# Kernel optimization log

Hardware: AMD Instinct MI355X
Metric: run time of the kernel (lower is better)

## Reference

```python
import jax, jax.numpy as jnp
import numpy as np

N_NODES = 100000
N_EDGES = 3200000
D_IN = 256
D_OUT = 256


def setup_inputs() -> dict:
    key = jax.random.key(0)
    k1, k2, k3, k4, k5 = jax.random.split(key, 5)
    inputs = jax.random.normal(k1, (N_NODES, D_IN), dtype=jnp.float32)
    # Glorot-uniform init as in _glorot_init
    init_range = np.sqrt(6.0 / (D_IN + D_OUT)).astype(np.float32)
    weight = jax.random.uniform(k2, (D_IN, D_OUT), dtype=jnp.float32,
                                minval=-init_range, maxval=init_range)
    edge_src = jax.random.randint(k3, (N_EDGES,), 0, N_NODES, dtype=jnp.int32)
    edge_dst = jax.random.randint(k4, (N_EDGES,), 0, N_NODES, dtype=jnp.int32)
    # normalized adjacency values (positive, like D^-1/2 A D^-1/2 entries)
    edge_vals = jax.random.uniform(k5, (N_EDGES,), dtype=jnp.float32)
    return {"inputs": inputs, "weight": weight, "edge_src": edge_src,
            "edge_dst": edge_dst, "edge_vals": edge_vals}


def reference(inputs, weight, edge_src, edge_dst, edge_vals):
    # x = inputs @ W          : [N, D_OUT]
    x = inputs @ weight
    # SpMM: out[d] = sum_{e: dst(e)=d} vals[e] * x[src(e)]
    msgs = edge_vals[:, None] * x[edge_src]          # [E, D_OUT]
    out = jax.ops.segment_sum(msgs, edge_dst, num_segments=inputs.shape[0])
    return jax.nn.relu(out)
```

## Files before the change

### kernel.cpp

```cpp
#include <hip/hip_runtime.h>

#define N_NODES 100000
#define N_EDGES 3200000
#define DDIM 256
#define NB 1563
#define BIN_BLK 256
#define CHUNK (N_EDGES / BIN_BLK)

typedef short s16x8 __attribute__((ext_vector_type(8)));
typedef float f32x4 __attribute__((ext_vector_type(4)));

__device__ __forceinline__ unsigned short f32_to_bf16(float f) {
    union { float f; unsigned int u; } c; c.f = f;
    unsigned int u = c.u;
    unsigned int r = u + 0x7fffu + ((u >> 16) & 1u);
    return (unsigned short)(r >> 16);
}
__device__ __forceinline__ float bf16_to_f32(unsigned short h) {
    union { unsigned int u; float f; } c; c.u = ((unsigned int)h) << 16;
    return c.f;
}

__global__ __launch_bounds__(256) void prep_w(const float* __restrict__ W,
                                              unsigned short* __restrict__ Wt) {
    __shared__ float tile[32][33];
    const int tx = threadIdx.x & 31;
    const int ty = threadIdx.x >> 5;
    const int n0 = blockIdx.x * 32;
    const int k0 = blockIdx.y * 32;
    for (int i = 0; i < 32; i += 8)
        tile[ty + i][tx] = W[(size_t)(k0 + ty + i) * DDIM + n0 + tx];
    __syncthreads();
    for (int i = 0; i < 32; i += 8)
        Wt[(size_t)(n0 + ty + i) * DDIM + k0 + tx] = f32_to_bf16(tile[tx][ty + i]);
}

__global__ __launch_bounds__(256) void gemm_mfma(const float* __restrict__ A,
                                                 const unsigned short* __restrict__ Wt,
                                                 unsigned short* __restrict__ Xb) {
    __shared__ unsigned short As[64][DDIM + 8];
    const int tid = threadIdx.x;
    const int rowBase = blockIdx.x * 64;

#pragma unroll
    for (int p = 0; p < 16; ++p) {
        const int flat = p * 256 + tid;
        const int row = flat >> 6;
        const int k4 = (flat & 63) * 4;
        const int gr = rowBase + row;
        float4 v = make_float4(0.f, 0.f, 0.f, 0.f);
        if (gr < N_NODES) v = *(const float4*)&A[(size_t)gr * DDIM + k4];
        ushort4 h;
        h.x = f32_to_bf16(v.x); h.y = f32_to_bf16(v.y);
        h.z = f32_to_bf16(v.z); h.w = f32_to_bf16(v.w);
        *(ushort4*)&As[row][k4] = h;
    }
    __syncthreads();

    const int wave = tid >> 6;
    const int lane = tid & 63;
    const int lrow = lane & 15;
    const int quad = lane >> 4;
    const int cb = wave * 64;

    f32x4 acc[4][4] = {};

#pragma unroll
    for (int ks = 0; ks < 8; ++ks) {
        const int k0 = ks * 32 + quad * 8;
        s16x8 a[4], b[4];
#pragma unroll
        for (int ri = 0; ri < 4; ++ri)
            a[ri] = *(const s16x8*)&As[ri * 16 + lrow][k0];
#pragma unroll
        for (int ci = 0; ci < 4; ++ci)
            b[ci] = *(const s16x8*)&Wt[(size_t)(cb + ci * 16 + lrow) * DDIM + k0];
#pragma unroll
        for (int ri = 0; ri < 4; ++ri)
#pragma unroll
            for (int ci = 0; ci < 4; ++ci)
                acc[ri][ci] = __builtin_amdgcn_mfma_f32_16x16x32_bf16(a[ri], b[ci], acc[ri][ci], 0, 0, 0);
    }

#pragma unroll
    for (int ri = 0; ri < 4; ++ri) {
        const int r0 = rowBase + ri * 16 + quad * 4;
#pragma unroll
        for (int rr = 0; rr < 4; ++rr) {
            const int row = r0 + rr;
            if (row < N_NODES) {
#pragma unroll
                for (int ci = 0; ci < 4; ++ci)
                    Xb[(size_t)row * DDIM + cb + ci * 16 + lrow] = f32_to_bf16(acc[ri][ci][rr]);
            }
        }
    }
}

__global__ __launch_bounds__(256) void zero_small(int* __restrict__ p, int n) {
    int i = blockIdx.x * 256 + threadIdx.x;
    if (i < n) p[i] = 0;
}

__global__ __launch_bounds__(256) void hist_coarse(const int* __restrict__ edst,
                                                   int* __restrict__ gcounts) {
    __shared__ int h[NB];
    const int tid = threadIdx.x;
    for (int i = tid; i < NB; i += 256) h[i] = 0;
    __syncthreads();
    const int lo = blockIdx.x * CHUNK;
    const int hi = lo + CHUNK;
    for (int e = lo + tid; e < hi; e += 256) atomicAdd(&h[edst[e] >> 6], 1);
    __syncthreads();
    for (int i = tid; i < NB; i += 256)
        if (h[i]) atomicAdd(&gcounts[i], h[i]);
}

__global__ __launch_bounds__(256) void scan_coarse(const int* __restrict__ gcounts,
                                                   int* __restrict__ bbase,
                                                   int* __restrict__ bcursor,
                                                   int* __restrict__ off) {
    __shared__ int part[256];
    const int t = threadIdx.x;
    const int chunk = (NB + 255) / 256;
    const int lo = t * chunk;
    const int hi = min(lo + chunk, NB);
    int s = 0;
    for (int i = lo; i < hi; ++i) s += gcounts[i];
    part[t] = s;
    __syncthreads();
    for (int d = 1; d < 256; d <<= 1) {
        int a = (t >= d) ? part[t - d] : 0;
        __syncthreads();
        part[t] += a;
        __syncthreads();
    }
    int run = part[t] - s;
    for (int i = lo; i < hi; ++i) {
        bbase[i] = run;
        bcursor[i] = run;
        run += gcounts[i];
    }
    if (t == 255) {
        bbase[NB] = run;
        off[N_NODES] = run;
    }
}

__global__ __launch_bounds__(256) void bin_coarse(const int* __restrict__ esrc,
                                                  const int* __restrict__ edst,
                                                  const float* __restrict__ evals,
                                                  int* __restrict__ bcursor,
                                                  int2* __restrict__ tmp) {
    __shared__ int h[NB];
    __shared__ int sb[NB];
    const int tid = threadIdx.x;
    for (int i = tid; i < NB; i += 256) h[i] = 0;
    __syncthreads();
    const int lo = blockIdx.x * CHUNK;
    const int hi = lo + CHUNK;
    for (int e = lo + tid; e < hi; e += 256) atomicAdd(&h[edst[e] >> 6], 1);
    __syncthreads();
    for (int i = tid; i < NB; i += 256)
        sb[i] = h[i] ? atomicAdd(&bcursor[i], h[i]) : 0;
    __syncthreads();
    for (int e = lo + tid; e < hi; e += 256) {
        const int d = edst[e];
        const int b = d >> 6;
        const int p = atomicAdd(&sb[b], 1);
        tmp[p] = make_int2(esrc[e] | ((d & 63) << 17), __float_as_int(evals[e]));
    }
}

__global__ __launch_bounds__(256) void refine(const int2* __restrict__ tmp,
                                              const int* __restrict__ bbase,
                                              int* __restrict__ off,
                                              int2* __restrict__ srcval) {
    __shared__ int nh[64];
    __shared__ int nb[64];
    const int b = blockIdx.x;
    const int tid = threadIdx.x;
    const int base = bbase[b];
    const int cnt = bbase[b + 1] - base;
    const int n0 = b * 64;
    const int nn = min(64, N_NODES - n0);
    if (tid < 64) nh[tid] = 0;
    __syncthreads();
    for (int i = tid; i < cnt; i += 256)
        atomicAdd(&nh[tmp[base + i].x >> 17], 1);
    __syncthreads();
    if (tid == 0) {
        int run = 0;
        for (int i = 0; i < 64; ++i) { nb[i] = run; run += nh[i]; }
    }
    __syncthreads();
    if (tid < nn) off[n0 + tid] = base + nb[tid];
    __syncthreads();
    for (int i = tid; i < cnt; i += 256) {
        const int2 r = tmp[base + i];
        const int dl = r.x >> 17;
        const int p = atomicAdd(&nb[dl], 1);
        srcval[base + p] = make_int2(r.x & 0x1FFFF, r.y);
    }
}

__global__ __launch_bounds__(256) void spmm_gather(const unsigned short* __restrict__ xb,
                                                   const int* __restrict__ off,
                                                   const int2* __restrict__ srcval,
                                                   float* __restrict__ out) {
    const int node = blockIdx.x * 4 + (threadIdx.x >> 6);
    const int lane = threadIdx.x & 63;
    const int start = off[node];
    const int end = off[node + 1];

    float4 acc = make_float4(0.f, 0.f, 0.f, 0.f);

    for (int base = start; base < end; base += 64) {
        const int cnt = min(64, end - base);
        int s_l = 0;
        float v_l = 0.f;
        if (lane < cnt) {
            int2 p = srcval[base + lane];
            s_l = p.x;
            v_l = __int_as_float(p.y);
        }
        int j = 0;
        for (; j + 4 <= cnt; j += 4) {
            const int s0 = __shfl(s_l, j + 0);
            const int s1 = __shfl(s_l, j + 1);
            const int s2 = __shfl(s_l, j + 2);
            const int s3 = __shfl(s_l, j + 3);
            const float v0 = __shfl(v_l, j + 0);
            const float v1 = __shfl(v_l, j + 1);
            const float v2 = __shfl(v_l, j + 2);
            const float v3 = __shfl(v_l, j + 3);
            const ushort4 h0 = *(const ushort4*)&xb[(size_t)s0 * DDIM + lane * 4];
            const ushort4 h1 = *(const ushort4*)&xb[(size_t)s1 * DDIM + lane * 4];
            const ushort4 h2 = *(const ushort4*)&xb[(size_t)s2 * DDIM + lane * 4];
            const ushort4 h3 = *(const ushort4*)&xb[(size_t)s3 * DDIM + lane * 4];
            acc.x += v0 * bf16_to_f32(h0.x); acc.y += v0 * bf16_to_f32(h0.y);
            acc.z += v0 * bf16_to_f32(h0.z); acc.w += v0 * bf16_to_f32(h0.w);
            acc.x += v1 * bf16_to_f32(h1.x); acc.y += v1 * bf16_to_f32(h1.y);
            acc.z += v1 * bf16_to_f32(h1.z); acc.w += v1 * bf16_to_f32(h1.w);
            acc.x += v2 * bf16_to_f32(h2.x); acc.y += v2 * bf16_to_f32(h2.y);
            acc.z += v2 * bf16_to_f32(h2.z); acc.w += v2 * bf16_to_f32(h2.w);
            acc.x += v3 * bf16_to_f32(h3.x); acc.y += v3 * bf16_to_f32(h3.y);
            acc.z += v3 * bf16_to_f32(h3.z); acc.w += v3 * bf16_to_f32(h3.w);
        }
        for (; j < cnt; ++j) {
            const int s = __shfl(s_l, j);
            const float v = __shfl(v_l, j);
            const ushort4 h = *(const ushort4*)&xb[(size_t)s * DDIM + lane * 4];
            acc.x += v * bf16_to_f32(h.x); acc.y += v * bf16_to_f32(h.y);
            acc.z += v * bf16_to_f32(h.z); acc.w += v * bf16_to_f32(h.w);
        }
    }

    acc.x = fmaxf(acc.x, 0.f);
    acc.y = fmaxf(acc.y, 0.f);
    acc.z = fmaxf(acc.z, 0.f);
    acc.w = fmaxf(acc.w, 0.f);
    *(float4*)&out[(size_t)node * DDIM + lane * 4] = acc;
}

extern "C" void kernel_launch(void* const* d_in, const int* in_sizes, int n_in,
                              void* d_out, int out_size, void* d_ws, size_t ws_size,
                              hipStream_t stream) {
    const float* inputs = (const float*)d_in[0];
    const float* weight = (const float*)d_in[1];
    const int* esrc     = (const int*)d_in[2];
    const int* edst     = (const int*)d_in[3];
    const float* evals  = (const float*)d_in[4];
    float* out = (float*)d_out;

    unsigned short* xb = (unsigned short*)d_ws;
    unsigned short* Wt = xb + (size_t)N_NODES * DDIM;
    int* off     = (int*)(Wt + DDIM * DDIM);
    int* gcounts = off + N_NODES + 1;
    int* bbase   = gcounts + NB;
    int* bcursor = bbase + NB + 1;
    uintptr_t a  = ((uintptr_t)(bcursor + NB) + 15) & ~(uintptr_t)15;
    int2* tmp    = (int2*)a;
    int2* srcval = tmp + N_EDGES;

    prep_w<<<dim3(8, 8), 256, 0, stream>>>(weight, Wt);

    gemm_mfma<<<(N_NODES + 63) / 64, 256, 0, stream>>>(inputs, Wt, xb);

    zero_small<<<(NB + 255) / 256, 256, 0, stream>>>(gcounts, NB);
    hist_coarse<<<BIN_BLK, 256, 0, stream>>>(edst, gcounts);
    scan_coarse<<<1, 256, 0, stream>>>(gcounts, bbase, bcursor, off);
    bin_coarse<<<BIN_BLK, 256, 0, stream>>>(esrc, edst, evals, bcursor, tmp);
    refine<<<NB, 256, 0, stream>>>(tmp, bbase, off, srcval);

    spmm_gather<<<N_NODES / 4, 256, 0, stream>>>(xb, off, srcval, out);
}
```

Measured before the change: 611.0 us.

## Fuse per-node refinement into SpMM, sorting bucket edges in shared memory

The separate refine pass, which wrote a node-sorted edge list to global memory, is removed. The SpMM kernel now loads each coarse bucket's edges, counting-sorts them by local destination in LDS with a wave-level scan, and gathers rows directly from shared memory. This removes a global write and reread of the edge list, the offsets array and one kernel launch. In exchange, each wave processes 16 nodes serially, and buckets larger than a fixed capacity would silently drop edges.

```diff
diff --git a/kernel.cpp b/kernel.cpp
--- a/kernel.cpp
+++ b/kernel.cpp
@@ -6,6 +6,7 @@
 #define NB 1563
 #define BIN_BLK 256
 #define CHUNK (N_EDGES / BIN_BLK)
+#define CAP 2560
 
 typedef short s16x8 __attribute__((ext_vector_type(8)));
 typedef float f32x4 __attribute__((ext_vector_type(4)));
@@ -16,9 +17,11 @@
     unsigned int r = u + 0x7fffu + ((u >> 16) & 1u);
     return (unsigned short)(r >> 16);
 }
-__device__ __forceinline__ float bf16_to_f32(unsigned short h) {
-    union { unsigned int u; float f; } c; c.u = ((unsigned int)h) << 16;
-    return c.f;
+__device__ __forceinline__ float bl16(unsigned int u) {
+    union { unsigned int x; float f; } c; c.x = u << 16; return c.f;
+}
+__device__ __forceinline__ float bh16(unsigned int u) {
+    union { unsigned int x; float f; } c; c.x = u & 0xffff0000u; return c.f;
 }
 
 __global__ __launch_bounds__(256) void prep_w(const float* __restrict__ W,
@@ -118,8 +121,7 @@
 
 __global__ __launch_bounds__(256) void scan_coarse(const int* __restrict__ gcounts,
                                                    int* __restrict__ bbase,
-                                                   int* __restrict__ bcursor,
-                                                   int* __restrict__ off) {
+                                                   int* __restrict__ bcursor) {
     __shared__ int part[256];
     const int t = threadIdx.x;
     const int chunk = (NB + 255) / 256;
@@ -141,10 +143,7 @@
         bcursor[i] = run;
         run += gcounts[i];
     }
-    if (t == 255) {
-        bbase[NB] = run;
-        off[N_NODES] = run;
-    }
+    if (t == 255) bbase[NB] = run;
 }
 
 __global__ __launch_bounds__(256) void bin_coarse(const int* __restrict__ esrc,
@@ -172,96 +171,93 @@
     }
 }
 
-__global__ __launch_bounds__(256) void refine(const int2* __restrict__ tmp,
-                                              const int* __restrict__ bbase,
-                                              int* __restrict__ off,
-                                              int2* __restrict__ srcval) {
+#define EDGE(q) { const float v = __int_as_float(r##q.y); \
+    a0 += v * bl16(h##q.x); a1 += v * bh16(h##q.x); \
+    a2 += v * bl16(h##q.y); a3 += v * bh16(h##q.y); }
+
+__global__ __launch_bounds__(256) void spmm_bucket(const unsigned short* __restrict__ xb,
+                                                   const int* __restrict__ bbase,
+                                                   const int2* __restrict__ tmp,
+                                                   float* __restrict__ out) {
+    __shared__ int2 sm[CAP];
     __shared__ int nh[64];
     __shared__ int nb[64];
+    __shared__ int soff[65];
+
     const int b = blockIdx.x;
     const int tid = threadIdx.x;
     const int base = bbase[b];
-    const int cnt = bbase[b + 1] - base;
-    const int n0 = b * 64;
-    const int nn = min(64, N_NODES - n0);
+    int cnt = bbase[b + 1] - base;
+    if (cnt > CAP) cnt = CAP;
+    const int n0 = b << 6;
+
     if (tid < 64) nh[tid] = 0;
     __syncthreads();
     for (int i = tid; i < cnt; i += 256)
-        atomicAdd(&nh[tmp[base + i].x >> 17], 1);
-    __syncthreads();
-    if (tid == 0) {
-        int run = 0;
-        for (int i = 0; i < 64; ++i) { nb[i] = run; run += nh[i]; }
-    }
-    __syncthreads();
-    if (tid < nn) off[n0 + tid] = base + nb[tid];
-    __syncthreads();
+        atomicAdd(&nh[(tmp[base + i].x >> 17) & 63], 1);
+    __syncthreads();
+
+    const int wave = tid >> 6;
+    const int lane = tid & 63;
+    if (wave == 0) {
+        const int x = nh[lane];
+        int inc = x;
+#pragma unroll
+        for (int d = 1; d < 64; d <<= 1) {
+            const int y = __shfl_up(inc, d);
+            if (lane >= d) inc += y;
+        }
+        soff[lane] = inc - x;
+        nb[lane] = inc - x;
+        if (lane == 63) soff[64] = inc;
+    }
+    __syncthreads();
+
     for (int i = tid; i < cnt; i += 256) {
         const int2 r = tmp[base + i];
-        const int dl = r.x >> 17;
-        const int p = atomicAdd(&nb[dl], 1);
-        srcval[base + p] = make_int2(r.x & 0x1FFFF, r.y);
-    }
-}
-
-__global__ __launch_bounds__(256) void spmm_gather(const unsigned short* __restrict__ xb,
-                                                   const int* __restrict__ off,
-                                                   const int2* __restrict__ srcval,
-                                                   float* __restrict__ out) {
-    const int node = blockIdx.x * 4 + (threadIdx.x >> 6);
-    const int lane = threadIdx.x & 63;
-    const int start = off[node];
-    const int end = off[node + 1];
-
-    float4 acc = make_float4(0.f, 0.f, 0.f, 0.f);
-
-    for (int base = start; base < end; base += 64) {
-        const int cnt = min(64, end - base);
-        int s_l = 0;
-        float v_l = 0.f;
-        if (lane < cnt) {
-            int2 p = srcval[base + lane];
-            s_l = p.x;
-            v_l = __int_as_float(p.y);
-        }
-        int j = 0;
-        for (; j + 4 <= cnt; j += 4) {
-            const int s0 = __shfl(s_l, j + 0);
-            const int s1 = __shfl(s_l, j + 1);
-            const int s2 = __shfl(s_l, j + 2);
-            const int s3 = __shfl(s_l, j + 3);
-            const float v0 = __shfl(v_l, j + 0);
-            const float v1 = __shfl(v_l, j + 1);
-            const float v2 = __shfl(v_l, j + 2);
-            const float v3 = __shfl(v_l, j + 3);
-            const ushort4 h0 = *(const ushort4*)&xb[(size_t)s0 * DDIM + lane * 4];
-            const ushort4 h1 = *(const ushort4*)&xb[(size_t)s1 * DDIM + lane * 4];
-            const ushort4 h2 = *(const ushort4*)&xb[(size_t)s2 * DDIM + lane * 4];
-            const ushort4 h3 = *(const ushort4*)&xb[(size_t)s3 * DDIM + lane * 4];
-            acc.x += v0 * bf16_to_f32(h0.x); acc.y += v0 * bf16_to_f32(h0.y);
-            acc.z += v0 * bf16_to_f32(h0.z); acc.w += v0 * bf16_to_f32(h0.w);
-            acc.x += v1 * bf16_to_f32(h1.x); acc.y += v1 * bf16_to_f32(h1.y);
-            acc.z += v1 * bf16_to_f32(h1.z); acc.w += v1 * bf16_to_f32(h1.w);
-            acc.x += v2 * bf16_to_f32(h2.x); acc.y += v2 * bf16_to_f32(h2.y);
-            acc.z += v2 * bf16_to_f32(h2.z); acc.w += v2 * bf16_to_f32(h2.w);
-            acc.x += v3 * bf16_to_f32(h3.x); acc.y += v3 * bf16_to_f32(h3.y);
-            acc.z += v3 * bf16_to_f32(h3.z); acc.w += v3 * bf16_to_f32(h3.w);
-        }
-        for (; j < cnt; ++j) {
-            const int s = __shfl(s_l, j);
-            const float v = __shfl(v_l, j);
-            const ushort4 h = *(const ushort4*)&xb[(size_t)s * DDIM + lane * 4];
-            acc.x += v * bf16_to_f32(h.x); acc.y += v * bf16_to_f32(h.y);
-            acc.z += v * bf16_to_f32(h.z); acc.w += v * bf16_to_f32(h.w);
-        }
-    }
-
-    acc.x = fmaxf(acc.x, 0.f);
-    acc.y = fmaxf(acc.y, 0.f);
-    acc.z = fmaxf(acc.z, 0.f);
-    acc.w = fmaxf(acc.w, 0.f);
-    *(float4*)&out[(size_t)node * DDIM + lane * 4] = acc;
-}
+        const int p = atomicAdd(&nb[(r.x >> 17) & 63], 1);
+        sm[p] = make_int2(r.x & 0x1FFFF, r.y);
+    }
+    __syncthreads();
+
+    const unsigned short* xcol = xb + (size_t)(lane << 2);
+    for (int dd = 0; dd < 16; ++dd) {
+        const int d = (wave << 4) + dd;
+        const int node = n0 + d;
+        if (node >= N_NODES) break;
+        int j = soff[d];
+        const int je = soff[d + 1];
+        float a0 = 0.f, a1 = 0.f, a2 = 0.f, a3 = 0.f;
+        for (; j + 8 <= je; j += 8) {
+            const int2 r0 = sm[j + 0]; const int2 r1 = sm[j + 1];
+            const int2 r2 = sm[j + 2]; const int2 r3 = sm[j + 3];
+            const int2 r4 = sm[j + 4]; const int2 r5 = sm[j + 5];
+            const int2 r6 = sm[j + 6]; const int2 r7 = sm[j + 7];
+            const uint2 h0 = *(const uint2*)&xcol[(size_t)r0.x * DDIM];
+            const uint2 h1 = *(const uint2*)&xcol[(size_t)r1.x * DDIM];
+            const uint2 h2 = *(const uint2*)&xcol[(size_t)r2.x * DDIM];
+            const uint2 h3 = *(const uint2*)&xcol[(size_t)r3.x * DDIM];
+            const uint2 h4 = *(const uint2*)&xcol[(size_t)r4.x * DDIM];
+            const uint2 h5 = *(const uint2*)&xcol[(size_t)r5.x * DDIM];
+            const uint2 h6 = *(const uint2*)&xcol[(size_t)r6.x * DDIM];
+            const uint2 h7 = *(const uint2*)&xcol[(size_t)r7.x * DDIM];
+            EDGE(0) EDGE(1) EDGE(2) EDGE(3)
+            EDGE(4) EDGE(5) EDGE(6) EDGE(7)
+        }
+        for (; j < je; ++j) {
+            const int2 r = sm[j];
+            const uint2 h = *(const uint2*)&xcol[(size_t)r.x * DDIM];
+            const float v = __int_as_float(r.y);
+            a0 += v * bl16(h.x); a1 += v * bh16(h.x);
+            a2 += v * bl16(h.y); a3 += v * bh16(h.y);
+        }
+        float4 o;
+        o.x = fmaxf(a0, 0.f); o.y = fmaxf(a1, 0.f);
+        o.z = fmaxf(a2, 0.f); o.w = fmaxf(a3, 0.f);
+        *(float4*)&out[(size_t)node * DDIM + (lane << 2)] = o;
+    }
+}
+#undef EDGE
 
 extern "C" void kernel_launch(void* const* d_in, const int* in_sizes, int n_in,
                               void* d_out, int out_size, void* d_ws, size_t ws_size,
@@ -275,13 +271,11 @@
 
     unsigned short* xb = (unsigned short*)d_ws;
     unsigned short* Wt = xb + (size_t)N_NODES * DDIM;
-    int* off     = (int*)(Wt + DDIM * DDIM);
-    int* gcounts = off + N_NODES + 1;
+    int* gcounts = (int*)(Wt + DDIM * DDIM);
     int* bbase   = gcounts + NB;
     int* bcursor = bbase + NB + 1;
     uintptr_t a  = ((uintptr_t)(bcursor + NB) + 15) & ~(uintptr_t)15;
     int2* tmp    = (int2*)a;
-    int2* srcval = tmp + N_EDGES;
 
     prep_w<<<dim3(8, 8), 256, 0, stream>>>(weight, Wt);
 
@@ -289,9 +283,8 @@
 
     zero_small<<<(NB + 255) / 256, 256, 0, stream>>>(gcounts, NB);
     hist_coarse<<<BIN_BLK, 256, 0, stream>>>(edst, gcounts);
-    scan_coarse<<<1, 256, 0, stream>>>(gcounts, bbase, bcursor, off);
+    scan_coarse<<<1, 256, 0, stream>>>(gcounts, bbase, bcursor);
     bin_coarse<<<BIN_BLK, 256, 0, stream>>>(esrc, edst, evals, bcursor, tmp);
-    refine<<<NB, 256, 0, stream>>>(tmp, bbase, off, srcval);
-
-    spmm_gather<<<N_NODES / 4, 256, 0, stream>>>(xb, off, srcval, out);
-}
+
+    spmm_bucket<<<NB, 256, 0, stream>>>(xb, bbase, tmp, out);
+}
```

New measurement: 613.1 us. Within noise of the previous version (+0.3%).

## Store X in 16-column panels and gather SpMM per panel

Applied to the files above, without the earlier changes.

The GEMM now writes the bf16 projected features into 16 column-panels (N×16 each) instead of row-major N×256. The SpMM is restructured so each block handles one panel for 64 destination nodes. Each wave processes 16 nodes, with 4 edge groups × 16 dims per lane, and reduces across lanes with shuffles. The aim is a per-panel working set (~3.2MB) that stays in cache during the random gathers. The cost is 16× re-reading of edge lists and offsets, 32-byte gathers per edge row, and narrow strided output stores.

```diff
diff --git a/kernel.cpp b/kernel.cpp
--- a/kernel.cpp
+++ b/kernel.cpp
@@ -6,6 +6,9 @@
 #define NB 1563
 #define BIN_BLK 256
 #define CHUNK (N_EDGES / BIN_BLK)
+#define PDIM 16
+#define NPANEL (DDIM / PDIM)
+#define PSTRIDE ((size_t)N_NODES * PDIM)
 
 typedef short s16x8 __attribute__((ext_vector_type(8)));
 typedef float f32x4 __attribute__((ext_vector_type(4)));
@@ -16,7 +19,7 @@
     unsigned int r = u + 0x7fffu + ((u >> 16) & 1u);
     return (unsigned short)(r >> 16);
 }
-__device__ __forceinline__ float bf16_to_f32(unsigned short h) {
+__device__ __forceinline__ float bf16s(unsigned short h) {
     union { unsigned int u; float f; } c; c.u = ((unsigned int)h) << 16;
     return c.f;
 }
@@ -91,7 +94,8 @@
             if (row < N_NODES) {
 #pragma unroll
                 for (int ci = 0; ci < 4; ++ci)
-                    Xb[(size_t)row * DDIM + cb + ci * 16 + lrow] = f32_to_bf16(acc[ri][ci][rr]);
+                    Xb[(size_t)(wave * 4 + ci) * PSTRIDE + (size_t)row * PDIM + lrow] =
+                        f32_to_bf16(acc[ri][ci][rr]);
             }
         }
     }
@@ -204,63 +208,55 @@
     }
 }
 
-__global__ __launch_bounds__(256) void spmm_gather(const unsigned short* __restrict__ xb,
-                                                   const int* __restrict__ off,
-                                                   const int2* __restrict__ srcval,
-                                                   float* __restrict__ out) {
-    const int node = blockIdx.x * 4 + (threadIdx.x >> 6);
+__global__ __launch_bounds__(256) void spmm_panel(const unsigned short* __restrict__ xb,
+                                                  const int* __restrict__ off,
+                                                  const int2* __restrict__ srcval,
+                                                  float* __restrict__ out) {
+    const int bp = blockIdx.x;
+    const int p  = bp / NB;
+    const int b  = bp - p * NB;
+    const int n0 = b << 6;
+    const int wave = threadIdx.x >> 6;
     const int lane = threadIdx.x & 63;
-    const int start = off[node];
-    const int end = off[node + 1];
-
-    float4 acc = make_float4(0.f, 0.f, 0.f, 0.f);
-
-    for (int base = start; base < end; base += 64) {
-        const int cnt = min(64, end - base);
-        int s_l = 0;
-        float v_l = 0.f;
-        if (lane < cnt) {
-            int2 p = srcval[base + lane];
-            s_l = p.x;
-            v_l = __int_as_float(p.y);
+    const int dim  = lane & 15;
+    const int es   = lane >> 4;
+
+    const unsigned short* xp = xb + (size_t)p * PSTRIDE + dim;
+
+    for (int dd = 0; dd < 16; ++dd) {
+        const int node = n0 + (wave << 4) + dd;
+        if (node >= N_NODES) break;
+        int j = off[node];
+        const int je = off[node + 1];
+        float acc0 = 0.f, acc1 = 0.f;
+        for (; j + 8 <= je; j += 8) {
+            const long long q0 = __builtin_nontemporal_load((const long long*)(srcval + j + es));
+            const long long q1 = __builtin_nontemporal_load((const long long*)(srcval + j + 4 + es));
+            const int s0 = (int)(q0 & 0x1FFFF);
+            const int s1 = (int)(q1 & 0x1FFFF);
+            const float v0 = __int_as_float((int)(q0 >> 32));
+            const float v1 = __int_as_float((int)(q1 >> 32));
+            const unsigned short x0 = xp[(size_t)s0 * PDIM];
+            const unsigned short x1 = xp[(size_t)s1 * PDIM];
+            acc0 += v0 * bf16s(x0);
+            acc1 += v1 * bf16s(x1);
         }
-        int j = 0;
-        for (; j + 4 <= cnt; j += 4) {
-            const int s0 = __shfl(s_l, j + 0);
-            const int s1 = __shfl(s_l, j + 1);
-            const int s2 = __shfl(s_l, j + 2);
-            const int s3 = __shfl(s_l, j + 3);
-            const float v0 = __shfl(v_l, j + 0);
-            const float v1 = __shfl(v_l, j + 1);
-            const float v2 = __shfl(v_l, j + 2);
-            const float v3 = __shfl(v_l, j + 3);
-            const ushort4 h0 = *(const ushort4*)&xb[(size_t)s0 * DDIM + lane * 4];
-            const ushort4 h1 = *(const ushort4*)&xb[(size_t)s1 * DDIM + lane * 4];
-            const ushort4 h2 = *(const ushort4*)&xb[(size_t)s2 * DDIM + lane * 4];
-            const ushort4 h3 = *(const ushort4*)&xb[(size_t)s3 * DDIM + lane * 4];
-            acc.x += v0 * bf16_to_f32(h0.x); acc.y += v0 * bf16_to_f32(h0.y);
-            acc.z += v0 * bf16_to_f32(h0.z); acc.w += v0 * bf16_to_f32(h0.w);
-            acc.x += v1 * bf16_to_f32(h1.x); acc.y += v1 * bf16_to_f32(h1.y);
-            acc.z += v1 * bf16_to_f32(h1.z); acc.w += v1 * bf16_to_f32(h1.w);
-            acc.x += v2 * bf16_to_f32(h2.x); acc.y += v2 * bf16_to_f32(h2.y);
-            acc.z += v2 * bf16_to_f32(h2.z); acc.w += v2 * bf16_to_f32(h2.w);
-            acc.x += v3 * bf16_to_f32(h3.x); acc.y += v3 * bf16_to_f32(h3.y);
-            acc.z += v3 * bf16_to_f32(h3.z); acc.w += v3 * bf16_to_f32(h3.w);
+        for (; j < je; j += 4) {
+            int s = 0; float v = 0.f;
+            if (j + es < je) {
+                const long long q = __builtin_nontemporal_load((const long long*)(srcval + j + es));
+                s = (int)(q & 0x1FFFF);
+                v = __int_as_float((int)(q >> 32));
+            }
+            const unsigned short x = xp[(size_t)s * PDIM];
+            acc0 += v * bf16s(x);
         }
-        for (; j < cnt; ++j) {
-            const int s = __shfl(s_l, j);
-            const float v = __shfl(v_l, j);
-            const ushort4 h = *(const ushort4*)&xb[(size_t)s * DDIM + lane * 4];
-            acc.x += v * bf16_to_f32(h.x); acc.y += v * bf16_to_f32(h.y);
-            acc.z += v * bf16_to_f32(h.z); acc.w += v * bf16_to_f32(h.w);
-        }
-    }
-
-    acc.x = fmaxf(acc.x, 0.f);
-    acc.y = fmaxf(acc.y, 0.f);
-    acc.z = fmaxf(acc.z, 0.f);
-    acc.w = fmaxf(acc.w, 0.f);
-    *(float4*)&out[(size_t)node * DDIM + lane * 4] = acc;
+        float acc = acc0 + acc1;
+        acc += __shfl_xor(acc, 16);
+        acc += __shfl_xor(acc, 32);
+        if (es == 0)
+            out[(size_t)node * DDIM + p * PDIM + dim] = fmaxf(acc, 0.f);
+    }
 }
 
 extern "C" void kernel_launch(void* const* d_in, const int* in_sizes, int n_in,
@@ -293,5 +289,5 @@
     bin_coarse<<<BIN_BLK, 256, 0, stream>>>(esrc, edst, evals, bcursor, tmp);
     refine<<<NB, 256, 0, stream>>>(tmp, bbase, off, srcval);
 
-    spmm_gather<<<N_NODES / 4, 256, 0, stream>>>(xb, off, srcval, out);
-}
+    spmm_panel<<<NB * NPANEL, 256, 0, stream>>>(xb, off, srcval, out);
+}
```

Measured after the change: 1.448 ms. 2.37x slower.
